# Optimization experiments

Hardware: AMD Instinct MI355X
Metric: run time of the kernel (lower is better)

Reference implementation:

```python
import jax, jax.numpy as jnp
import numpy as np
import math

N_HEADS = 16

def setup_inputs() -> dict:
    key = jax.random.key(0)
    k1, k2, k3 = jax.random.split(key, 3)
    B, S, D = 2, 2048, 1024
    x = jax.random.normal(k1, (B, S, D), dtype=jnp.float32)
    qkv = 0.01 * jax.random.normal(k2, (3 * D, D), dtype=jnp.float32)
    wo = 0.01 * jax.random.normal(k3, (D, D), dtype=jnp.float32)
    return {"x": x, "qkv": qkv, "wo": wo}

def reference(x, qkv, wo):
    B, S, D = x.shape
    H = N_HEADS
    dh = D // H
    QKV = x @ qkv.T                      # [B,S,3D]
    Q, K, V = jnp.split(QKV, 3, axis=-1)
    q = Q.reshape(B, S, H, dh).transpose(0, 2, 1, 3)  # [B,H,S,dh]
    k = K.reshape(B, S, H, dh).transpose(0, 2, 1, 3)
    v = V.reshape(B, S, H, dh).transpose(0, 2, 1, 3)
    scores = jnp.einsum('bhqd,bhkd->bhqk', q, k) / math.sqrt(float(dh))
    # Faithful to original: multiply by lower-triangular mask, then set
    # exact zeros to -inf (masked positions become 0 then -inf).
    mask = jnp.tril(jnp.ones((S, S), dtype=scores.dtype))
    scores = scores * mask[None, None, :, :]
    scores = jnp.where(scores == 0, -jnp.inf, scores)
    attn = jax.nn.softmax(scores, axis=-1)
    out = jnp.einsum('bhqk,bhkd->bhqd', attn, v)       # [B,H,S,dh]
    out = out.transpose(0, 2, 1, 3).reshape(B, S, D)
    return out @ wo.T
```

## Files before the change

kernel.cpp:

```cpp
#include <hip/hip_runtime.h>

typedef unsigned short u16;
typedef unsigned int u32;
typedef __bf16 bf16x8 __attribute__((ext_vector_type(8)));
typedef float f32x4 __attribute__((ext_vector_type(4)));
typedef u16 u16x4 __attribute__((ext_vector_type(4)));

#define GL2LDS16(g, l)                                                         \
    __builtin_amdgcn_global_load_lds(                                          \
        (__attribute__((address_space(1))) const void*)(g),                    \
        (__attribute__((address_space(3))) void*)(l), 16, 0, 0)

#define SYNC_VM(n) asm volatile("s_waitcnt vmcnt(" #n ")\ns_barrier" ::: "memory")
#define BAR()      asm volatile("s_barrier" ::: "memory")

__device__ __forceinline__ u16 f2bf(float f) {
    union { float f; u32 u; } x; x.f = f;
    u32 r = x.u + 0x7FFFu + ((x.u >> 16) & 1u);
    return (u16)(r >> 16);
}

__device__ __forceinline__ u32 pack2bf(float f0, float f1) {
    union { float f; u32 u; } a, b;
    a.f = f0; b.f = f1;
    return __builtin_amdgcn_perm(b.u + 0x8000u, a.u + 0x8000u, 0x07060302u);
}

__device__ __forceinline__ float fast_exp2(float x) {
    float r;
    asm("v_exp_f32 %0, %1" : "=v"(r) : "v"(x));
    return r;
}

__device__ __forceinline__ bf16x8 scale_frag(bf16x8 v) {
#pragma unroll
    for (int i = 0; i < 8; ++i) v[i] = (__bf16)((float)v[i] * 0.1803368801f);
    return v;
}

__global__ __launch_bounds__(256) void convert_all_kernel(const float* __restrict__ x,
                                                          const float* __restrict__ qkv,
                                                          const float* __restrict__ wo,
                                                          u16* __restrict__ out) {
    int i = (blockIdx.x * 256 + threadIdx.x) * 4;
    const float* src;
    int off;
    if (i < 4194304)      { src = x;   off = i; }
    else if (i < 7340032) { src = qkv; off = i - 4194304; }
    else                  { src = wo;  off = i - 7340032; }
    float4 v = *(const float4*)(src + off);
    u16x4 o;
    o.x = f2bf(v.x); o.y = f2bf(v.y); o.z = f2bf(v.z); o.w = f2bf(v.w);
    *(u16x4*)(out + i) = o;
}

template <int TM, bool OUT_BF16, bool FUSE_VT>
__global__ __launch_bounds__(256) void gemm_bt(const u16* __restrict__ A,
                                               const u16* __restrict__ B,
                                               void* __restrict__ Cout,
                                               u16* __restrict__ VtG,
                                               int M, int N, int K) {
    constexpr int MI = TM / 32;
    __shared__ u16 As[2][TM * 32];
    __shared__ u16 Bs[2][128 * 32];
    const int tid = threadIdx.x;
    const int w = tid >> 6, lane = tid & 63, ln = lane & 15, qd = lane >> 4;
    const int wr = w >> 1, wc = w & 1;
    const int m0 = blockIdx.y * TM, n0 = blockIdx.x * 128;

    const int srow = tid >> 2, scol = (tid & 3) * 8;
    const u16* Abase = A + (size_t)(m0 + srow) * K + scol;
    const u16* Bbase = B + (size_t)(n0 + srow) * K + scol;

    f32x4 acc[MI][4] = {};
    const int nsteps = K >> 5;

#pragma unroll
    for (int it = 0; it < TM / 64; ++it)
        GL2LDS16(Abase + (size_t)(it * 64) * K, &As[0][(tid + it * 256) * 8]);
#pragma unroll
    for (int it = 0; it < 2; ++it)
        GL2LDS16(Bbase + (size_t)(it * 64) * K, &Bs[0][(tid + it * 256) * 8]);

    for (int s = 0; s < nsteps; ++s) {
        const u16* Ab = As[s & 1];
        const u16* Bb = Bs[s & 1];
        if (s + 1 < nsteps) {
            const int nk = (s + 1) << 5;
            const int nb = (s + 1) & 1;
#pragma unroll
            for (int it = 0; it < TM / 64; ++it)
                GL2LDS16(Abase + (size_t)(it * 64) * K + nk, &As[nb][(tid + it * 256) * 8]);
#pragma unroll
            for (int it = 0; it < 2; ++it)
                GL2LDS16(Bbase + (size_t)(it * 64) * K + nk, &Bs[nb][(tid + it * 256) * 8]);
            if constexpr (TM == 128) SYNC_VM(4); else SYNC_VM(3);
        } else {
            SYNC_VM(0);
        }

        bf16x8 af[MI], bfr[4];
#pragma unroll
        for (int i = 0; i < MI; ++i)
            af[i] = *(const bf16x8*)&Ab[(wr * (TM / 2) + i * 16 + ln) * 32 + qd * 8];
#pragma unroll
        for (int j = 0; j < 4; ++j)
            bfr[j] = *(const bf16x8*)&Bb[(wc * 64 + j * 16 + ln) * 32 + qd * 8];
#pragma unroll
        for (int i = 0; i < MI; ++i)
#pragma unroll
            for (int j = 0; j < 4; ++j)
                acc[i][j] = __builtin_amdgcn_mfma_f32_16x16x32_bf16(af[i], bfr[j], acc[i][j], 0, 0, 0);
        BAR();
    }

    if (FUSE_VT && n0 >= 2048) {
        const int bq = m0 >> 11;
        const int sl = (m0 & 2047) + wr * (TM / 2) + qd * 4;
#pragma unroll
        for (int i = 0; i < MI; ++i)
#pragma unroll
            for (int j = 0; j < 4; ++j) {
                int d = n0 - 2048 + wc * 64 + j * 16 + ln;
                int vrow = (bq * 16 + (d >> 6)) * 64 + (d & 63);
                u16x4 ov;
                ov.x = f2bf(acc[i][j][0]); ov.y = f2bf(acc[i][j][1]);
                ov.z = f2bf(acc[i][j][2]); ov.w = f2bf(acc[i][j][3]);
                *(u16x4*)&VtG[(size_t)vrow * 2048 + sl + i * 16] = ov;
            }
        return;
    }

#pragma unroll
    for (int i = 0; i < MI; ++i)
#pragma unroll
        for (int j = 0; j < 4; ++j)
#pragma unroll
            for (int r = 0; r < 4; ++r) {
                int row = m0 + wr * (TM / 2) + i * 16 + qd * 4 + r;
                int col = n0 + wc * 64 + j * 16 + ln;
                float v = acc[i][j][r];
                if constexpr (OUT_BF16)
                    ((u16*)Cout)[(size_t)row * N + col] = f2bf(v);
                else
                    ((float*)Cout)[(size_t)row * N + col] = v;
            }
}

__global__ __launch_bounds__(256) void attn_kernel(const u16* __restrict__ QKV,
                                                   const u16* __restrict__ VtG,
                                                   u16* __restrict__ AO) {
    __shared__ u16 Ks[2][64 * 64];
    __shared__ u16 Vts[2][64 * 64];
    __shared__ u16 Pls[4][16 * 64];

    const int tid = threadIdx.x;
    const int w = tid >> 6, lane = tid & 63, ln = lane & 15, qd = lane >> 4;
    const int b = blockIdx.z, h = blockIdx.y;
    const int t = blockIdx.x;
    const int tH = 63 - t, tL = t;
    const int tile = (w < 2) ? tH : tL;
    const int myq = tile * 32 + (w & 1) * 16 + ln;
    const int bh = b * 16 + h;
    const int swz = ln & 7;
    const int nchH = (tH >> 1) + 1;
    const int mynch = (tile >> 1) + 1;

    const int sr0 = tid >> 3;
    const int sg = (tid & 7) ^ (sr0 & 7);
    const u16* ksrc = QKV + (size_t)(b * 2048 + sr0) * 3072 + 1024 + h * 64 + sg * 8;
    const u16* vsrc = VtG + (size_t)(bh * 64 + sr0) * 2048 + sg * 8;

    GL2LDS16(ksrc, &Ks[0][tid * 8]);
    GL2LDS16(ksrc + (size_t)32 * 3072, &Ks[0][tid * 8 + 2048]);
    GL2LDS16(vsrc, &Vts[0][tid * 8]);
    GL2LDS16(vsrc + (size_t)32 * 2048, &Vts[0][tid * 8 + 2048]);

    const u16* qp = QKV + (size_t)(b * 2048 + myq) * 3072 + h * 64;
    bf16x8 qf0 = scale_frag(*(const bf16x8*)(qp + qd * 8));
    bf16x8 qf1 = scale_frag(*(const bf16x8*)(qp + 32 + qd * 8));

    f32x4 o[4] = {};
    float l = 0.f;
    u16* Pw = Pls[w];

    for (int c = 0; c < nchH; ++c) {
        if (c + 1 < nchH) {
            const int k1 = (c + 1) * 64;
            const int nb = (c + 1) & 1;
            GL2LDS16(ksrc + (size_t)k1 * 3072, &Ks[nb][tid * 8]);
            GL2LDS16(ksrc + (size_t)(k1 + 32) * 3072, &Ks[nb][tid * 8 + 2048]);
            GL2LDS16(vsrc + k1, &Vts[nb][tid * 8]);
            GL2LDS16(vsrc + k1 + 32 * 2048, &Vts[nb][tid * 8 + 2048]);
            SYNC_VM(4);
        } else {
            SYNC_VM(0);
        }

        if (c < mynch) {
            const u16* Kb = Ks[c & 1];
            const u16* Vb = Vts[c & 1];

            f32x4 s[4];
#pragma unroll
            for (int kt = 0; kt < 4; ++kt) {
                const u16* kr = Kb + (kt * 16 + ln) * 64;
                bf16x8 kf0 = *(const bf16x8*)(kr + ((qd ^ swz) * 8));
                bf16x8 kf1 = *(const bf16x8*)(kr + (((qd + 4) ^ swz) * 8));
                f32x4 z = {0.f, 0.f, 0.f, 0.f};
                z = __builtin_amdgcn_mfma_f32_16x16x32_bf16(kf0, qf0, z, 0, 0, 0);
                z = __builtin_amdgcn_mfma_f32_16x16x32_bf16(kf1, qf1, z, 0, 0, 0);
                s[kt] = z;
            }

            if (c == mynch - 1) {
#pragma unroll
                for (int kt = 0; kt < 4; ++kt)
#pragma unroll
                    for (int r = 0; r < 4; ++r) {
                        int key = c * 64 + kt * 16 + qd * 4 + r;
                        if (key > myq) s[kt][r] = -1e30f;
                    }
            }
#pragma unroll
            for (int kt = 0; kt < 4; ++kt) {
                float p0 = fast_exp2(s[kt][0]), p1 = fast_exp2(s[kt][1]);
                float p2 = fast_exp2(s[kt][2]), p3 = fast_exp2(s[kt][3]);
                l += (p0 + p1) + (p2 + p3);
                uint2 pk = {pack2bf(p0, p1), pack2bf(p2, p3)};
                int g = kt * 2 + (qd >> 1);
                *(uint2*)&Pw[ln * 64 + ((g ^ swz) * 8) + (qd & 1) * 4] = pk;
            }
            bf16x8 pf0 = *(const bf16x8*)&Pw[ln * 64 + ((qd ^ swz) * 8)];
            bf16x8 pf1 = *(const bf16x8*)&Pw[ln * 64 + (((qd + 4) ^ swz) * 8)];

#pragma unroll
            for (int dt = 0; dt < 4; ++dt) {
                const u16* vr = Vb + (dt * 16 + ln) * 64;
                bf16x8 vf0 = *(const bf16x8*)(vr + ((qd ^ swz) * 8));
                bf16x8 vf1 = *(const bf16x8*)(vr + (((qd + 4) ^ swz) * 8));
                o[dt] = __builtin_amdgcn_mfma_f32_16x16x32_bf16(vf0, pf0, o[dt], 0, 0, 0);
                o[dt] = __builtin_amdgcn_mfma_f32_16x16x32_bf16(vf1, pf1, o[dt], 0, 0, 0);
            }
        }
        BAR();
    }

    l += __shfl_xor(l, 16); l += __shfl_xor(l, 32);
    float inv = 1.0f / l;
#pragma unroll
    for (int dt = 0; dt < 4; ++dt) {
        uint2 ov = {pack2bf(o[dt][0] * inv, o[dt][1] * inv),
                    pack2bf(o[dt][2] * inv, o[dt][3] * inv)};
        *(uint2*)&AO[(size_t)(b * 2048 + myq) * 1024 + h * 64 + dt * 16 + qd * 4] = ov;
    }
}

extern "C" void kernel_launch(void* const* d_in, const int* in_sizes, int n_in,
                              void* d_out, int out_size, void* d_ws, size_t ws_size,
                              hipStream_t stream) {
    const float* x   = (const float*)d_in[0];
    const float* qkv = (const float*)d_in[1];
    const float* wo  = (const float*)d_in[2];
    float* out = (float*)d_out;

    char* ws = (char*)d_ws;
    u16* xb    = (u16*)(ws + 0);
    u16* qkvb  = (u16*)(ws + 8388608);
    u16* wob   = (u16*)(ws + 14680064);
    u16* QKVo  = (u16*)(ws + 16777216);
    u16* AO    = (u16*)(ws + 41943040);
    u16* VtG   = (u16*)(ws + 50331648);

    convert_all_kernel<<<8192, 256, 0, stream>>>(x, qkv, wo, xb);

    gemm_bt<128, true, true><<<dim3(24, 32), 256, 0, stream>>>(xb, qkvb, QKVo, VtG,
                                                               4096, 3072, 1024);

    attn_kernel<<<dim3(32, 16, 2), 256, 0, stream>>>(QKVo, VtG, AO);

    gemm_bt<64, false, false><<<dim3(8, 64), 256, 0, stream>>>(AO, wob, out, nullptr,
                                                               4096, 1024, 1024);
}
```

Before: 181.9 us.

## Use 32x32 MFMA in attention with register-resident P and split-key wave pairs

Reworks the attention kernel to use 32x32x16 bf16 MFMAs. Each wave now covers 32 queries instead of 16, and the K rows are permuted on load so the QK^T accumulator layout matches the PV B-operand, letting P stay in registers without an LDS round trip. Pairs of waves split the key chunks by parity, then merge partial O and l through LDS scratch at the end. It also adds s_setprio around MFMA sections. The cost is larger accumulators, a final reduction barrier, and each wave doing half the chunks, which may hurt load balance.

```diff
diff --git a/kernel.cpp b/kernel.cpp
--- a/kernel.cpp
+++ b/kernel.cpp
@@ -4,6 +4,7 @@
 typedef unsigned int u32;
 typedef __bf16 bf16x8 __attribute__((ext_vector_type(8)));
 typedef float f32x4 __attribute__((ext_vector_type(4)));
+typedef float f32x16 __attribute__((ext_vector_type(16)));
 typedef u16 u16x4 __attribute__((ext_vector_type(4)));
 
 #define GL2LDS16(g, l)                                                         \
@@ -152,23 +153,23 @@
                                                    u16* __restrict__ AO) {
     __shared__ u16 Ks[2][64 * 64];
     __shared__ u16 Vts[2][64 * 64];
-    __shared__ u16 Pls[4][16 * 64];
 
     const int tid = threadIdx.x;
-    const int w = tid >> 6, lane = tid & 63, ln = lane & 15, qd = lane >> 4;
+    const int w = tid >> 6, lane = tid & 63;
+    const int q = lane & 31, hi = lane >> 5, swz = q & 7;
     const int b = blockIdx.z, h = blockIdx.y;
     const int t = blockIdx.x;
-    const int tH = 63 - t, tL = t;
-    const int tile = (w < 2) ? tH : tL;
-    const int myq = tile * 32 + (w & 1) * 16 + ln;
+    const int tile = (w < 2) ? (63 - t) : t;
+    const int myq = tile * 32 + q;
     const int bh = b * 16 + h;
-    const int swz = ln & 7;
-    const int nchH = (tH >> 1) + 1;
+    const int nchH = ((63 - t) >> 1) + 1;
     const int mynch = (tile >> 1) + 1;
+    const int par = (w ^ (h >> 3) ^ b) & 1;
 
     const int sr0 = tid >> 3;
+    const int srP = (sr0 & 19) | ((sr0 & 4) << 1) | ((sr0 & 8) >> 1);
     const int sg = (tid & 7) ^ (sr0 & 7);
-    const u16* ksrc = QKV + (size_t)(b * 2048 + sr0) * 3072 + 1024 + h * 64 + sg * 8;
+    const u16* ksrc = QKV + (size_t)(b * 2048 + srP) * 3072 + 1024 + h * 64 + sg * 8;
     const u16* vsrc = VtG + (size_t)(bh * 64 + sr0) * 2048 + sg * 8;
 
     GL2LDS16(ksrc, &Ks[0][tid * 8]);
@@ -177,12 +178,13 @@
     GL2LDS16(vsrc + (size_t)32 * 2048, &Vts[0][tid * 8 + 2048]);
 
     const u16* qp = QKV + (size_t)(b * 2048 + myq) * 3072 + h * 64;
-    bf16x8 qf0 = scale_frag(*(const bf16x8*)(qp + qd * 8));
-    bf16x8 qf1 = scale_frag(*(const bf16x8*)(qp + 32 + qd * 8));
-
-    f32x4 o[4] = {};
+    bf16x8 qf[4];
+#pragma unroll
+    for (int ks = 0; ks < 4; ++ks)
+        qf[ks] = scale_frag(*(const bf16x8*)(qp + ks * 16 + hi * 8));
+
+    f32x16 o0 = {}, o1 = {};
     float l = 0.f;
-    u16* Pw = Pls[w];
 
     for (int c = 0; c < nchH; ++c) {
         if (c + 1 < nchH) {
@@ -197,62 +199,81 @@
             SYNC_VM(0);
         }
 
-        if (c < mynch) {
+        if (((c & 1) == par) && c < mynch) {
             const u16* Kb = Ks[c & 1];
             const u16* Vb = Vts[c & 1];
-
-            f32x4 s[4];
-#pragma unroll
-            for (int kt = 0; kt < 4; ++kt) {
-                const u16* kr = Kb + (kt * 16 + ln) * 64;
-                bf16x8 kf0 = *(const bf16x8*)(kr + ((qd ^ swz) * 8));
-                bf16x8 kf1 = *(const bf16x8*)(kr + (((qd + 4) ^ swz) * 8));
-                f32x4 z = {0.f, 0.f, 0.f, 0.f};
-                z = __builtin_amdgcn_mfma_f32_16x16x32_bf16(kf0, qf0, z, 0, 0, 0);
-                z = __builtin_amdgcn_mfma_f32_16x16x32_bf16(kf1, qf1, z, 0, 0, 0);
-                s[kt] = z;
+            bf16x8 pa[4];
+
+#pragma unroll
+            for (int kb = 0; kb < 2; ++kb) {
+                f32x16 z = {};
+                __builtin_amdgcn_s_setprio(1);
+#pragma unroll
+                for (int ks = 0; ks < 4; ++ks) {
+                    bf16x8 kf = *(const bf16x8*)&Kb[(kb * 32 + q) * 64 + (((ks * 2 + hi) ^ swz) * 8)];
+                    z = __builtin_amdgcn_mfma_f32_32x32x16_bf16(kf, qf[ks], z, 0, 0, 0);
+                }
+                __builtin_amdgcn_s_setprio(0);
+
+                if (c == mynch - 1) {
+#pragma unroll
+                    for (int r = 0; r < 16; ++r) {
+                        int key = c * 64 + kb * 32 + (r & 3) + 4 * ((r >> 2) & 1)
+                                  + 8 * hi + 16 * (r >> 3);
+                        if (key > myq) z[r] = -1e30f;
+                    }
+                }
+
+#pragma unroll
+                for (int r = 0; r < 16; ++r) {
+                    float p = fast_exp2(z[r]);
+                    l += p;
+                    pa[kb * 2 + (r >> 3)][4 * ((r >> 2) & 1) + (r & 3)] = (__bf16)p;
+                }
             }
 
-            if (c == mynch - 1) {
-#pragma unroll
-                for (int kt = 0; kt < 4; ++kt)
-#pragma unroll
-                    for (int r = 0; r < 4; ++r) {
-                        int key = c * 64 + kt * 16 + qd * 4 + r;
-                        if (key > myq) s[kt][r] = -1e30f;
-                    }
+            __builtin_amdgcn_s_setprio(1);
+#pragma unroll
+            for (int ks = 0; ks < 4; ++ks) {
+                bf16x8 vf0 = *(const bf16x8*)&Vb[q * 64 + (((ks * 2 + hi) ^ swz) * 8)];
+                bf16x8 vf1 = *(const bf16x8*)&Vb[(32 + q) * 64 + (((ks * 2 + hi) ^ swz) * 8)];
+                o0 = __builtin_amdgcn_mfma_f32_32x32x16_bf16(vf0, pa[ks], o0, 0, 0, 0);
+                o1 = __builtin_amdgcn_mfma_f32_32x32x16_bf16(vf1, pa[ks], o1, 0, 0, 0);
             }
-#pragma unroll
-            for (int kt = 0; kt < 4; ++kt) {
-                float p0 = fast_exp2(s[kt][0]), p1 = fast_exp2(s[kt][1]);
-                float p2 = fast_exp2(s[kt][2]), p3 = fast_exp2(s[kt][3]);
-                l += (p0 + p1) + (p2 + p3);
-                uint2 pk = {pack2bf(p0, p1), pack2bf(p2, p3)};
-                int g = kt * 2 + (qd >> 1);
-                *(uint2*)&Pw[ln * 64 + ((g ^ swz) * 8) + (qd & 1) * 4] = pk;
-            }
-            bf16x8 pf0 = *(const bf16x8*)&Pw[ln * 64 + ((qd ^ swz) * 8)];
-            bf16x8 pf1 = *(const bf16x8*)&Pw[ln * 64 + (((qd + 4) ^ swz) * 8)];
-
-#pragma unroll
-            for (int dt = 0; dt < 4; ++dt) {
-                const u16* vr = Vb + (dt * 16 + ln) * 64;
-                bf16x8 vf0 = *(const bf16x8*)(vr + ((qd ^ swz) * 8));
-                bf16x8 vf1 = *(const bf16x8*)(vr + (((qd + 4) ^ swz) * 8));
-                o[dt] = __builtin_amdgcn_mfma_f32_16x16x32_bf16(vf0, pf0, o[dt], 0, 0, 0);
-                o[dt] = __builtin_amdgcn_mfma_f32_16x16x32_bf16(vf1, pf1, o[dt], 0, 0, 0);
-            }
+            __builtin_amdgcn_s_setprio(0);
         }
         BAR();
     }
 
-    l += __shfl_xor(l, 16); l += __shfl_xor(l, 32);
-    float inv = 1.0f / l;
-#pragma unroll
-    for (int dt = 0; dt < 4; ++dt) {
-        uint2 ov = {pack2bf(o[dt][0] * inv, o[dt][1] * inv),
-                    pack2bf(o[dt][2] * inv, o[dt][3] * inv)};
-        *(uint2*)&AO[(size_t)(b * 2048 + myq) * 1024 + h * 64 + dt * 16 + qd * 4] = ov;
+    l += __shfl_xor(l, 32);
+    float* scrO = (float*)&Ks[0][0];
+    float* scrL = (float*)&Vts[0][0];
+    const int slot = w >> 1;
+    if (par == 1) {
+#pragma unroll
+        for (int j = 0; j < 4; ++j) {
+            f32x4 s0 = {o0[4 * j + 0], o0[4 * j + 1], o0[4 * j + 2], o0[4 * j + 3]};
+            *(f32x4*)&scrO[slot * 2048 + lane * 32 + ((j ^ (lane & 7)) * 4)] = s0;
+            f32x4 s1 = {o1[4 * j + 0], o1[4 * j + 1], o1[4 * j + 2], o1[4 * j + 3]};
+            *(f32x4*)&scrO[slot * 2048 + lane * 32 + (((j + 4) ^ (lane & 7)) * 4)] = s1;
+        }
+        scrL[slot * 64 + lane] = l;
+    }
+    BAR();
+    if (par == 0) {
+        l += scrL[slot * 64 + lane];
+        float inv = 1.0f / l;
+#pragma unroll
+        for (int j = 0; j < 4; ++j) {
+            f32x4 s0 = *(const f32x4*)&scrO[slot * 2048 + lane * 32 + ((j ^ (lane & 7)) * 4)];
+            f32x4 s1 = *(const f32x4*)&scrO[slot * 2048 + lane * 32 + (((j + 4) ^ (lane & 7)) * 4)];
+            uint2 ov0 = {pack2bf((o0[4 * j + 0] + s0.x) * inv, (o0[4 * j + 1] + s0.y) * inv),
+                         pack2bf((o0[4 * j + 2] + s0.z) * inv, (o0[4 * j + 3] + s0.w) * inv)};
+            *(uint2*)&AO[(size_t)(b * 2048 + myq) * 1024 + h * 64 + 8 * j + 4 * hi] = ov0;
+            uint2 ov1 = {pack2bf((o1[4 * j + 0] + s1.x) * inv, (o1[4 * j + 1] + s1.y) * inv),
+                         pack2bf((o1[4 * j + 2] + s1.z) * inv, (o1[4 * j + 3] + s1.w) * inv)};
+            *(uint2*)&AO[(size_t)(b * 2048 + myq) * 1024 + h * 64 + 32 + 8 * j + 4 * hi] = ov1;
+        }
     }
 }
 
```

Measured after the change: 222.9 us. +22.5%, slower.

## Stage fused V-transpose epilogue through LDS and raise priority around MFMA blocks

Applied to the files above, without the earlier changes.

The fused QKV GEMM epilogue now writes the V tile into a shared-memory buffer with XOR swizzling and reads it back as 16-byte vectors. This turns the transposed V store from scattered 8-byte writes into contiguous 16-byte global stores. It also wraps the MFMA sequences in the GEMM and attention kernels with s_setprio to favour matrix issue across waves. The cost is extra LDS traffic and barriers in the epilogue. The epilogue hardcodes wr*64, so it assumes TM=128.

```diff
diff --git a/kernel.cpp b/kernel.cpp
--- a/kernel.cpp
+++ b/kernel.cpp
@@ -5,6 +5,7 @@
 typedef __bf16 bf16x8 __attribute__((ext_vector_type(8)));
 typedef float f32x4 __attribute__((ext_vector_type(4)));
 typedef u16 u16x4 __attribute__((ext_vector_type(4)));
+typedef u16 u16x8 __attribute__((ext_vector_type(8)));
 
 #define GL2LDS16(g, l)                                                         \
     __builtin_amdgcn_global_load_lds(                                          \
@@ -13,6 +14,7 @@
 
 #define SYNC_VM(n) asm volatile("s_waitcnt vmcnt(" #n ")\ns_barrier" ::: "memory")
 #define BAR()      asm volatile("s_barrier" ::: "memory")
+#define BAR_DS()   asm volatile("s_waitcnt lgkmcnt(0)\ns_barrier" ::: "memory")
 
 __device__ __forceinline__ u16 f2bf(float f) {
     union { float f; u32 u; } x; x.f = f;
@@ -61,8 +63,9 @@
                                                u16* __restrict__ VtG,
                                                int M, int N, int K) {
     constexpr int MI = TM / 32;
-    __shared__ u16 As[2][TM * 32];
-    __shared__ u16 Bs[2][128 * 32];
+    __shared__ u16 SM[2 * TM * 32 + 2 * 128 * 32];
+    u16* Asm = SM;
+    u16* Bsm = SM + 2 * TM * 32;
     const int tid = threadIdx.x;
     const int w = tid >> 6, lane = tid & 63, ln = lane & 15, qd = lane >> 4;
     const int wr = w >> 1, wc = w & 1;
@@ -77,23 +80,23 @@
 
 #pragma unroll
     for (int it = 0; it < TM / 64; ++it)
-        GL2LDS16(Abase + (size_t)(it * 64) * K, &As[0][(tid + it * 256) * 8]);
+        GL2LDS16(Abase + (size_t)(it * 64) * K, &Asm[(tid + it * 256) * 8]);
 #pragma unroll
     for (int it = 0; it < 2; ++it)
-        GL2LDS16(Bbase + (size_t)(it * 64) * K, &Bs[0][(tid + it * 256) * 8]);
+        GL2LDS16(Bbase + (size_t)(it * 64) * K, &Bsm[(tid + it * 256) * 8]);
 
     for (int s = 0; s < nsteps; ++s) {
-        const u16* Ab = As[s & 1];
-        const u16* Bb = Bs[s & 1];
+        const u16* Ab = &Asm[(s & 1) * TM * 32];
+        const u16* Bb = &Bsm[(s & 1) * 128 * 32];
         if (s + 1 < nsteps) {
             const int nk = (s + 1) << 5;
             const int nb = (s + 1) & 1;
 #pragma unroll
             for (int it = 0; it < TM / 64; ++it)
-                GL2LDS16(Abase + (size_t)(it * 64) * K + nk, &As[nb][(tid + it * 256) * 8]);
+                GL2LDS16(Abase + (size_t)(it * 64) * K + nk, &Asm[nb * TM * 32 + (tid + it * 256) * 8]);
 #pragma unroll
             for (int it = 0; it < 2; ++it)
-                GL2LDS16(Bbase + (size_t)(it * 64) * K + nk, &Bs[nb][(tid + it * 256) * 8]);
+                GL2LDS16(Bbase + (size_t)(it * 64) * K + nk, &Bsm[nb * 128 * 32 + (tid + it * 256) * 8]);
             if constexpr (TM == 128) SYNC_VM(4); else SYNC_VM(3);
         } else {
             SYNC_VM(0);
@@ -106,29 +109,45 @@
 #pragma unroll
         for (int j = 0; j < 4; ++j)
             bfr[j] = *(const bf16x8*)&Bb[(wc * 64 + j * 16 + ln) * 32 + qd * 8];
+        __builtin_amdgcn_s_setprio(1);
 #pragma unroll
         for (int i = 0; i < MI; ++i)
 #pragma unroll
             for (int j = 0; j < 4; ++j)
                 acc[i][j] = __builtin_amdgcn_mfma_f32_16x16x32_bf16(af[i], bfr[j], acc[i][j], 0, 0, 0);
+        __builtin_amdgcn_s_setprio(0);
         BAR();
     }
 
-    if (FUSE_VT && n0 >= 2048) {
-        const int bq = m0 >> 11;
-        const int sl = (m0 & 2047) + wr * (TM / 2) + qd * 4;
-#pragma unroll
-        for (int i = 0; i < MI; ++i)
-#pragma unroll
-            for (int j = 0; j < 4; ++j) {
-                int d = n0 - 2048 + wc * 64 + j * 16 + ln;
+    if constexpr (FUSE_VT) {
+        if (n0 >= 2048) {
+            const int bq = m0 >> 11;
+            BAR_DS();
+#pragma unroll
+            for (int i = 0; i < MI; ++i)
+#pragma unroll
+                for (int j = 0; j < 4; ++j) {
+                    int col = wc * 64 + j * 16 + ln;
+                    int row0 = wr * 64 + i * 16 + qd * 4;
+                    int pr = row0 ^ (((col >> 2) & 3) << 4);
+                    u16x4 ov;
+                    ov.x = f2bf(acc[i][j][0]); ov.y = f2bf(acc[i][j][1]);
+                    ov.z = f2bf(acc[i][j][2]); ov.w = f2bf(acc[i][j][3]);
+                    *(u16x4*)&SM[col * 128 + pr] = ov;
+                }
+            BAR_DS();
+#pragma unroll
+            for (int p = 0; p < 8; ++p) {
+                int flat = p * 2048 + tid * 8;
+                int colL = flat >> 7, rowL = flat & 127;
+                int pr = rowL ^ (((colL >> 2) & 3) << 4);
+                u16x8 v = *(const u16x8*)&SM[colL * 128 + pr];
+                int d = n0 - 2048 + colL;
                 int vrow = (bq * 16 + (d >> 6)) * 64 + (d & 63);
-                u16x4 ov;
-                ov.x = f2bf(acc[i][j][0]); ov.y = f2bf(acc[i][j][1]);
-                ov.z = f2bf(acc[i][j][2]); ov.w = f2bf(acc[i][j][3]);
-                *(u16x4*)&VtG[(size_t)vrow * 2048 + sl + i * 16] = ov;
-            }
-        return;
+                *(u16x8*)&VtG[(size_t)vrow * 2048 + (m0 & 2047) + rowL] = v;
+            }
+            return;
+        }
     }
 
 #pragma unroll
@@ -202,6 +221,7 @@
             const u16* Vb = Vts[c & 1];
 
             f32x4 s[4];
+            __builtin_amdgcn_s_setprio(1);
 #pragma unroll
             for (int kt = 0; kt < 4; ++kt) {
                 const u16* kr = Kb + (kt * 16 + ln) * 64;
@@ -212,6 +232,7 @@
                 z = __builtin_amdgcn_mfma_f32_16x16x32_bf16(kf1, qf1, z, 0, 0, 0);
                 s[kt] = z;
             }
+            __builtin_amdgcn_s_setprio(0);
 
             if (c == mynch - 1) {
 #pragma unroll
@@ -234,6 +255,7 @@
             bf16x8 pf0 = *(const bf16x8*)&Pw[ln * 64 + ((qd ^ swz) * 8)];
             bf16x8 pf1 = *(const bf16x8*)&Pw[ln * 64 + (((qd + 4) ^ swz) * 8)];
 
+            __builtin_amdgcn_s_setprio(1);
 #pragma unroll
             for (int dt = 0; dt < 4; ++dt) {
                 const u16* vr = Vb + (dt * 16 + ln) * 64;
@@ -242,6 +264,7 @@
                 o[dt] = __builtin_amdgcn_mfma_f32_16x16x32_bf16(vf0, pf0, o[dt], 0, 0, 0);
                 o[dt] = __builtin_amdgcn_mfma_f32_16x16x32_bf16(vf1, pf1, o[dt], 0, 0, 0);
             }
+            __builtin_amdgcn_s_setprio(0);
         }
         BAR();
     }
```

Result: faster. 175.3 us (-3.6%).
